# Performance work log

Hardware: AMD Instinct MI355X
Metric: run time of the kernel (lower is better)

The kernel has to match this reference:

```python
import jax, jax.numpy as jnp
import numpy as np

N, E = 100000, 1600000          # nodes, edges
DIN, DH, DOUT = 128, 128, 64    # input_dim, hidden_dim, output_dim


def setup_inputs() -> dict:
    key = jax.random.key(0)
    k0, k1, k2, k3 = jax.random.split(key, 4)
    x = jax.random.normal(k0, (N, DIN), dtype=jnp.float32)
    edge_index = jax.random.randint(k1, (2, E), 0, N)
    # GCNConv params (glorot-ish weights, zero bias)
    W1 = jax.random.normal(k2, (DIN, DH), dtype=jnp.float32) / np.sqrt(DIN).astype(np.float32)
    b1 = jnp.zeros((DH,), jnp.float32)
    W2 = jax.random.normal(k3, (DH, DOUT), dtype=jnp.float32) / np.sqrt(DH).astype(np.float32)
    b2 = jnp.zeros((DOUT,), jnp.float32)
    return {"x": x, "edge_index": edge_index, "W1": W1, "b1": b1, "W2": W2, "b2": b2}


def _gcn_conv(h_in, W, b, src, dst, norm_e, self_norm, n):
    # PyG GCNConv: transform, then normalized sum-aggregation with self-loops.
    h = h_in @ W                                   # [N, dout]
    msg = h[src] * norm_e[:, None]                 # [E, dout] gather + edge scale
    agg = jax.ops.segment_sum(msg, dst, num_segments=n)
    agg = agg + h * self_norm[:, None]             # self-loop contribution (norm = 1/deg)
    return agg + b


def reference(x, edge_index, W1, b1, W2, b2):
    src, dst = edge_index[0], edge_index[1]
    n = x.shape[0]
    # degree including self-loop, computed on dst (PyG convention)
    deg = jax.ops.segment_sum(jnp.ones((src.shape[0],), x.dtype), dst, num_segments=n) + 1.0
    dinv = jax.lax.rsqrt(deg)
    norm_e = dinv[src] * dinv[dst]                 # per-edge D^-1/2 A D^-1/2
    self_norm = dinv * dinv
    h = _gcn_conv(x, W1, b1, src, dst, norm_e, self_norm, n)
    h = jax.nn.relu(h)                             # dropout is identity in eval mode
    out = _gcn_conv(h, W2, b2, src, dst, norm_e, self_norm, n)
    return out
```

## Files before the change

### kernel.cpp

```cpp
#include <hip/hip_runtime.h>

#define NN 100000
#define NE 1600000
#define NBUCK 1563
#define NBH 256
#define CHUNK 6250
#define NSEG 8
#define SEGC (NBH/NSEG)
#define NBXB 12500
#define NBG 1563


typedef short bf16x8 __attribute__((ext_vector_type(8)));
typedef float f32x4  __attribute__((ext_vector_type(4)));
typedef float f32x2  __attribute__((ext_vector_type(2)));

__device__ __forceinline__ float b2f(unsigned short u) {
    return __uint_as_float(((unsigned int)u) << 16);
}
__device__ __forceinline__ unsigned short f2b(float f) {
    unsigned int x = __float_as_uint(f);
    x += 0x7FFFu + ((x >> 16) & 1u);
    return (unsigned short)(x >> 16);
}

__global__ __launch_bounds__(256) void k_pre(const float* __restrict__ x,
                                             unsigned short* __restrict__ xb,
                                             const int* __restrict__ dst,
                                             int* __restrict__ ghist) {
    int b = blockIdx.x;
    if (b < NBXB) {
        int id = b * 256 + threadIdx.x;
        float4 v = ((const float4*)x)[id];
        ushort4 o;
        o.x = f2b(v.x); o.y = f2b(v.y); o.z = f2b(v.z); o.w = f2b(v.w);
        ((ushort4*)xb)[id] = o;
        return;
    }
    __shared__ int h[NBUCK];
    int tid = threadIdx.x;
    int i = b - NBXB;
    for (int k = tid; k < NBUCK; k += 256) h[k] = 0;
    __syncthreads();
    int e0 = i * CHUNK;
    for (int e = e0 + tid; e < e0 + CHUNK; e += 256) {
        unsigned d = (unsigned)dst[e];
        if (d < NN) atomicAdd(&h[d >> 6], 1);
    }
    __syncthreads();
    for (int k = tid; k < NBUCK; k += 256) ghist[i * NBUCK + k] = h[k];
}

__global__ __launch_bounds__(256) void k_scanB(const int* __restrict__ ghist,
                                               int* __restrict__ boffT,
                                               int* __restrict__ tot) {
    __shared__ int part[NSEG][32];
    int kk = threadIdx.x & 31, seg = threadIdx.x >> 5;
    int k = blockIdx.x * 32 + kk;
    bool ok = (k < NBUCK);
    int i0 = seg * SEGC;
    int S = 0;
    if (ok) {
#pragma unroll 8
        for (int i = i0; i < i0 + SEGC; ++i) S += ghist[i * NBUCK + k];
    }
    part[seg][kk] = S;
    __syncthreads();
    int pre = 0;
#pragma unroll
    for (int s2 = 0; s2 < NSEG; ++s2) pre += (s2 < seg) ? part[s2][kk] : 0;
    if (ok) {
        int run = pre;
#pragma unroll 8
        for (int i = i0; i < i0 + SEGC; ++i) {
            int c = ghist[i * NBUCK + k];
            boffT[i * NBUCK + k] = run;
            run += c;
        }
        if (seg == NSEG - 1) tot[k] = run;
    }
}

__global__ __launch_bounds__(256) void k_place(const int* __restrict__ src,
                                               const int* __restrict__ dst,
                                               const int* __restrict__ tot,
                                               const int* __restrict__ boffT,
                                               int* __restrict__ ebuf,
                                               int* __restrict__ bbase_out) {
    __shared__ int cur[NBUCK];
    __shared__ int s[256];
    const int tid = threadIdx.x, bid = blockIdx.x;
    const int i = ((bid & 7) * (NBH / 8)) + (bid >> 3);
    int k0 = tid * 7;
    int v[7]; int S = 0;
#pragma unroll
    for (int q = 0; q < 7; ++q) {
        int k = k0 + q;
        v[q] = (k < NBUCK) ? tot[k] : 0;
        S += v[q];
    }
    s[tid] = S;
    __syncthreads();
    for (int off = 1; off < 256; off <<= 1) {
        int t = (tid >= off) ? s[tid - off] : 0;
        __syncthreads();
        s[tid] += t;
        __syncthreads();
    }
    int run = s[tid] - S;
#pragma unroll
    for (int q = 0; q < 7; ++q) {
        int k = k0 + q;
        if (k < NBUCK) {
            cur[k] = run + boffT[i * NBUCK + k];
            if (bid == 0) bbase_out[k] = run;
            run += v[q];
        }
    }
    __syncthreads();
    int e0 = i * CHUNK;
    for (int e = e0 + tid; e < e0 + CHUNK; e += 256) {
        unsigned d = (unsigned)dst[e];
        if (d >= NN) continue;
        unsigned sv = (unsigned)src[e];
        if (sv >= NN) sv = 0;
        int pos = atomicAdd(&cur[d >> 6], 1);
        ebuf[pos] = (int)(sv | ((d & 63u) << 17));
    }
}

__global__ __launch_bounds__(256) void k_binC(const int* __restrict__ bbase,
                                              const int* __restrict__ tot,
                                              const int* __restrict__ ebuf,
                                              int* __restrict__ row_start,
                                              float* __restrict__ dinv,
                                              int* __restrict__ csr) {
    __shared__ int cnt[64], excl[64], cur[64];
    int b = blockIdx.x, tid = threadIdx.x;
    int n0 = b * 64;
    int base = bbase[b], end = base + tot[b];
    if (tid < 64) cnt[tid] = 0;
    __syncthreads();
    for (int i = base + tid; i < end; i += 256)
        atomicAdd(&cnt[((unsigned)ebuf[i]) >> 17], 1);
    __syncthreads();
    if (tid == 0) {
        int run = 0;
        for (int t = 0; t < 64; ++t) { excl[t] = run; run += cnt[t]; }
    }
    __syncthreads();
    if (tid < 64) {
        int node = n0 + tid;
        if (node < NN) {
            row_start[node] = base + excl[tid];
            dinv[node] = rsqrtf((float)cnt[tid] + 1.0f);
        }
        cur[tid] = base + excl[tid];
    }
    if (b == NBUCK - 1 && tid == 0) row_start[NN] = end;
    __syncthreads();
    for (int i = base + tid; i < end; i += 256) {
        unsigned rec = (unsigned)ebuf[i];
        int pos = atomicAdd(&cur[rec >> 17], 1);
        csr[pos] = (int)(rec & 0x1FFFFu);
    }
}

__global__ __launch_bounds__(256) void k_agg1(const unsigned short* __restrict__ xb,
                                              const float* __restrict__ dinv,
                                              const int* __restrict__ row_start,
                                              const int* __restrict__ csr,
                                              char* __restrict__ P) {
    int node = blockIdx.x * 4 + (threadIdx.x >> 6);
    int lane = threadIdx.x & 63;
    int sub  = lane >> 4;
    int dimb = lane & 15;
    const uint4* X4 = (const uint4*)xb;
    float dv = dinv[node];
    float sn4 = dv * dv * 0.25f;
    uint4 sv = X4[(size_t)node * 16 + dimb];
    f32x2 a0, a1, a2, a3;
    a0.x = __uint_as_float(sv.x << 16) * sn4;  a0.y = __uint_as_float(sv.x & 0xFFFF0000u) * sn4;
    a1.x = __uint_as_float(sv.y << 16) * sn4;  a1.y = __uint_as_float(sv.y & 0xFFFF0000u) * sn4;
    a2.x = __uint_as_float(sv.z << 16) * sn4;  a2.y = __uint_as_float(sv.z & 0xFFFF0000u) * sn4;
    a3.x = __uint_as_float(sv.w << 16) * sn4;  a3.y = __uint_as_float(sv.w & 0xFFFF0000u) * sn4;
    int base = row_start[node], end = row_start[node + 1];
    for (int c0 = base; c0 < end; c0 += 64) {
        int idx = c0 + lane;
        int cl = min(idx, end - 1);
        int s = csr[cl];
        float wv = (idx < end) ? dinv[s] * dv : 0.f;
        int ng = min(64, end - c0);
        for (int g = 0; g * 4 < ng; ++g) {
            int   sq = __shfl(s,  g * 4 + sub);
            float wq = __shfl(wv, g * 4 + sub);
            uint4 v = X4[(size_t)sq * 16 + dimb];
            f32x2 wv2; wv2.x = wq; wv2.y = wq;
            f32x2 xv;
            xv.x = __uint_as_float(v.x << 16); xv.y = __uint_as_float(v.x & 0xFFFF0000u);
            a0 = __builtin_elementwise_fma(xv, wv2, a0);
            xv.x = __uint_as_float(v.y << 16); xv.y = __uint_as_float(v.y & 0xFFFF0000u);
            a1 = __builtin_elementwise_fma(xv, wv2, a1);
            xv.x = __uint_as_float(v.z << 16); xv.y = __uint_as_float(v.z & 0xFFFF0000u);
            a2 = __builtin_elementwise_fma(xv, wv2, a2);
            xv.x = __uint_as_float(v.w << 16); xv.y = __uint_as_float(v.w & 0xFFFF0000u);
            a3 = __builtin_elementwise_fma(xv, wv2, a3);
        }
    }
#pragma unroll
    for (int mgap = 16; mgap < 64; mgap <<= 1) {
        a0.x += __shfl_xor(a0.x, mgap); a0.y += __shfl_xor(a0.y, mgap);
        a1.x += __shfl_xor(a1.x, mgap); a1.y += __shfl_xor(a1.y, mgap);
        a2.x += __shfl_xor(a2.x, mgap); a2.y += __shfl_xor(a2.y, mgap);
        a3.x += __shfl_xor(a3.x, mgap); a3.y += __shfl_xor(a3.y, mgap);
    }
    if (lane < 16) {
        uint4 o;
        o.x = (unsigned)f2b(a0.x) | ((unsigned)f2b(a0.y) << 16);
        o.y = (unsigned)f2b(a1.x) | ((unsigned)f2b(a1.y) << 16);
        o.z = (unsigned)f2b(a2.x) | ((unsigned)f2b(a2.y) << 16);
        o.w = (unsigned)f2b(a3.x) | ((unsigned)f2b(a3.y) << 16);
        ((uint4*)(P + (size_t)node * 256))[lane] = o;
    }
}

__global__ __launch_bounds__(256) void k_gemm12(const float* __restrict__ W1,
                                                const float* __restrict__ b1,
                                                const float* __restrict__ W2,
                                                char* __restrict__ P) {
    __shared__ short Wl1[16384];
    __shared__ short Wl2[8192];
    __shared__ __align__(16) short Cl[4][16][128];
    const int tid = threadIdx.x;
    const int w = tid >> 6, lane = tid & 63;
    const int r0 = blockIdx.x * 64;

    for (int i = tid; i < 16384; i += 256) {
        int j = i & 7, l = (i >> 3) & 63, ks = (i >> 9) & 3, ct = i >> 11;
        int k = ks * 32 + ((l >> 4) << 3) + j;
        int c = ct * 16 + (l & 15);
        Wl1[i] = (short)f2b(W1[k * 128 + c]);
    }
    for (int i = tid; i < 8192; i += 256) {
        int j = i & 7, l = (i >> 3) & 63, ks = (i >> 9) & 3, ct = i >> 11;
        int k = ks * 32 + ((l >> 4) << 3) + j;
        int c = ct * 16 + (l & 15);
        Wl2[i] = (short)f2b(W2[k * 64 + c]);
    }
    __syncthreads();

    const int m = r0 + w * 16 + (lane & 15);
    const int quad = lane >> 4;
    const bool mok = (m < NN);
    bf16x8 a[4];
#pragma unroll
    for (int ks = 0; ks < 4; ++ks) {
        if (mok) a[ks] = *(const bf16x8*)(P + (size_t)m * 256 + (ks * 32 + quad * 8) * 2);
        else     a[ks] = bf16x8{0,0,0,0,0,0,0,0};
    }
#pragma unroll
    for (int ct = 0; ct < 8; ++ct) {
        f32x4 c = {0.f, 0.f, 0.f, 0.f};
#pragma unroll
        for (int ks = 0; ks < 4; ++ks) {
            bf16x8 b = *(const bf16x8*)&Wl1[((ct * 4 + ks) * 64 + lane) * 8];
            c = __builtin_amdgcn_mfma_f32_16x16x32_bf16(a[ks], b, c, 0, 0, 0);
        }
        int col = ct * 16 + (lane & 15);
        float bias = b1[col];
#pragma unroll
        for (int r = 0; r < 4; ++r)
            Cl[w][quad * 4 + r][col] = (short)f2b(fmaxf(c[r] + bias, 0.f));
    }
    __syncthreads();
    bf16x8 a2[4];
#pragma unroll
    for (int ks = 0; ks < 4; ++ks)
        a2[ks] = *(const bf16x8*)&Cl[w][lane & 15][ks * 32 + quad * 8];
    __syncthreads();
    short* Ct = &Cl[0][0][0];
#pragma unroll
    for (int ct = 0; ct < 4; ++ct) {
        f32x4 c = {0.f, 0.f, 0.f, 0.f};
#pragma unroll
        for (int ks = 0; ks < 4; ++ks) {
            bf16x8 b = *(const bf16x8*)&Wl2[((ct * 4 + ks) * 64 + lane) * 8];
            c = __builtin_amdgcn_mfma_f32_16x16x32_bf16(a2[ks], b, c, 0, 0, 0);
        }
        int col = ct * 16 + (lane & 15);
#pragma unroll
        for (int r = 0; r < 4; ++r)
            Ct[(w * 16 + quad * 4 + r) * 64 + col] = (short)f2b(c[r]);
    }
    __syncthreads();
    for (int it = 0; it < 8; ++it) {
        int row = it * 2 + (lane >> 5), u = lane & 31;
        int node = r0 + w * 16 + row;
        if (node < NN)
            *(unsigned int*)(P + (size_t)node * 256 + u * 4) =
                ((const unsigned int*)&Ct[(w * 16 + row) * 64])[u];
    }
}

__global__ __launch_bounds__(256) void k_agg2(const float* __restrict__ dinv,
                                              const int* __restrict__ row_start,
                                              const int* __restrict__ csr,
                                              const char* __restrict__ P,
                                              const float* __restrict__ b2,
                                              float* __restrict__ outp) {
    int node = blockIdx.x * 4 + (threadIdx.x >> 6);
    int lane = threadIdx.x & 63;
    int sub  = lane >> 3;
    int dimb = lane & 7;
    const uint4* P4 = (const uint4*)P;
    float dv = dinv[node];
    float sn8 = dv * dv * 0.125f;
    uint4 sv = P4[(size_t)node * 16 + dimb];
    f32x2 a0, a1, a2, a3;
    a0.x = __uint_as_float(sv.x << 16) * sn8;  a0.y = __uint_as_float(sv.x & 0xFFFF0000u) * sn8;
    a1.x = __uint_as_float(sv.y << 16) * sn8;  a1.y = __uint_as_float(sv.y & 0xFFFF0000u) * sn8;
    a2.x = __uint_as_float(sv.z << 16) * sn8;  a2.y = __uint_as_float(sv.z & 0xFFFF0000u) * sn8;
    a3.x = __uint_as_float(sv.w << 16) * sn8;  a3.y = __uint_as_float(sv.w & 0xFFFF0000u) * sn8;
    int base = row_start[node], end = row_start[node + 1];
    if (end > base) {
        for (int c0 = base; c0 < end; c0 += 64) {
            int idx = c0 + lane;
            int cl = min(idx, end - 1);
            int s = csr[cl];
            float wv = (idx < end) ? dinv[s] * dv : 0.f;
            int ng = min(64, end - c0);
            for (int g = 0; g * 8 < ng; ++g) {
                int   sq = __shfl(s,  g * 8 + sub);
                float wq = __shfl(wv, g * 8 + sub);
                uint4 v = P4[(size_t)sq * 16 + dimb];
                f32x2 wv2; wv2.x = wq; wv2.y = wq;
                f32x2 xv;
                xv.x = __uint_as_float(v.x << 16); xv.y = __uint_as_float(v.x & 0xFFFF0000u);
                a0 = __builtin_elementwise_fma(xv, wv2, a0);
                xv.x = __uint_as_float(v.y << 16); xv.y = __uint_as_float(v.y & 0xFFFF0000u);
                a1 = __builtin_elementwise_fma(xv, wv2, a1);
                xv.x = __uint_as_float(v.z << 16); xv.y = __uint_as_float(v.z & 0xFFFF0000u);
                a2 = __builtin_elementwise_fma(xv, wv2, a2);
                xv.x = __uint_as_float(v.w << 16); xv.y = __uint_as_float(v.w & 0xFFFF0000u);
                a3 = __builtin_elementwise_fma(xv, wv2, a3);
            }
        }
    }
#pragma unroll
    for (int mgap = 8; mgap < 64; mgap <<= 1) {
        a0.x += __shfl_xor(a0.x, mgap); a0.y += __shfl_xor(a0.y, mgap);
        a1.x += __shfl_xor(a1.x, mgap); a1.y += __shfl_xor(a1.y, mgap);
        a2.x += __shfl_xor(a2.x, mgap); a2.y += __shfl_xor(a2.y, mgap);
        a3.x += __shfl_xor(a3.x, mgap); a3.y += __shfl_xor(a3.y, mgap);
    }
    if (lane < 8) {
        float4 ba = ((const float4*)b2)[lane * 2];
        float4 bb = ((const float4*)b2)[lane * 2 + 1];
        float4 o0, o1;
        o0.x = a0.x + ba.x; o0.y = a0.y + ba.y; o0.z = a1.x + ba.z; o0.w = a1.y + ba.w;
        o1.x = a2.x + bb.x; o1.y = a2.y + bb.y; o1.z = a3.x + bb.z; o1.w = a3.y + bb.w;
        ((float4*)outp)[(size_t)node * 16 + lane * 2]     = o0;
        ((float4*)outp)[(size_t)node * 16 + lane * 2 + 1] = o1;
    }
}

extern "C" void kernel_launch(void* const* d_in, const int* in_sizes, int n_in,
                              void* d_out, int out_size, void* d_ws, size_t ws_size,
                              hipStream_t stream) {
    const float* x  = (const float*)d_in[0];
    const int*   ei = (const int*)d_in[1];
    const float* W1 = (const float*)d_in[2];
    const float* b1 = (const float*)d_in[3];
    const float* W2 = (const float*)d_in[4];
    const float* b2 = (const float*)d_in[5];
    float* out = (float*)d_out;
    const int* src = ei;
    const int* dst = ei + NE;

    char* ws = (char*)d_ws;
    unsigned short* xb        = (unsigned short*)(ws + 0);
    char*           P         = ws + 25600000;
    int*            ghist     = (int*)(ws + 25600000);
    int*            boffT     = (int*)(ws + 27200512);
    int*            tot       = (int*)(ws + 28801024);
    int*            bbase     = (int*)(ws + 28807276);
    int*            row_start = (int*)(ws + 51200000);
    float*          dinv      = (float*)(ws + 51600004);
    int*            csr       = (int*)(ws + 52000004);
    int*            ebuf      = (int*)(ws + 58400004);

    k_pre  <<<NBXB + NBH, 256, 0, stream>>>(x, xb, dst, ghist);
    k_scanB<<<(NBUCK + 31) / 32, 256, 0, stream>>>(ghist, boffT, tot);
    k_place<<<NBH, 256, 0, stream>>>(src, dst, tot, boffT, ebuf, bbase);
    k_binC <<<NBUCK, 256, 0, stream>>>(bbase, tot, ebuf, row_start, dinv, csr);

    k_agg1  <<<NN / 4, 256, 0, stream>>>(xb, dinv, row_start, csr, P);
    k_gemm12<<<NBG, 256, 0, stream>>>(W1, b1, W2, P);
    k_agg2  <<<NN / 4, 256, 0, stream>>>(dinv, row_start, csr, P, b2, out);
}
```

Baseline: 311.9 us.

## Make fused GEMM kernel persistent to amortize per-block weight staging

```diff
diff --git a/kernel.cpp b/kernel.cpp
--- a/kernel.cpp
+++ b/kernel.cpp
@@ -9,6 +9,7 @@
 #define SEGC (NBH/NSEG)
 #define NBXB 12500
 #define NBG 1563
+#define NBGG 512
 
 
 typedef short bf16x8 __attribute__((ext_vector_type(8)));
@@ -230,10 +231,10 @@
                                                 char* __restrict__ P) {
     __shared__ short Wl1[16384];
     __shared__ short Wl2[8192];
-    __shared__ __align__(16) short Cl[4][16][128];
+    __shared__ __align__(16) short Cl[4][16][136];
     const int tid = threadIdx.x;
     const int w = tid >> 6, lane = tid & 63;
-    const int r0 = blockIdx.x * 64;
+    const int quad = lane >> 4, l15 = lane & 15;
 
     for (int i = tid; i < 16384; i += 256) {
         int j = i & 7, l = (i >> 3) & 63, ks = (i >> 9) & 3, ct = i >> 11;
@@ -247,58 +248,56 @@
         int c = ct * 16 + (l & 15);
         Wl2[i] = (short)f2b(W2[k * 64 + c]);
     }
-    __syncthreads();
-
-    const int m = r0 + w * 16 + (lane & 15);
-    const int quad = lane >> 4;
-    const bool mok = (m < NN);
-    bf16x8 a[4];
-#pragma unroll
-    for (int ks = 0; ks < 4; ++ks) {
-        if (mok) a[ks] = *(const bf16x8*)(P + (size_t)m * 256 + (ks * 32 + quad * 8) * 2);
-        else     a[ks] = bf16x8{0,0,0,0,0,0,0,0};
-    }
-#pragma unroll
-    for (int ct = 0; ct < 8; ++ct) {
-        f32x4 c = {0.f, 0.f, 0.f, 0.f};
+    float bias1[8];
+#pragma unroll
+    for (int ct = 0; ct < 8; ++ct) bias1[ct] = b1[ct * 16 + l15];
+    __syncthreads();
+
+    for (int t = blockIdx.x; t < NBG; t += NBGG) {
+        const int r0 = t * 64;
+        const int m = r0 + w * 16 + l15;
+        const bool mok = (m < NN);
+        bf16x8 a[4];
 #pragma unroll
         for (int ks = 0; ks < 4; ++ks) {
-            bf16x8 b = *(const bf16x8*)&Wl1[((ct * 4 + ks) * 64 + lane) * 8];
-            c = __builtin_amdgcn_mfma_f32_16x16x32_bf16(a[ks], b, c, 0, 0, 0);
-        }
-        int col = ct * 16 + (lane & 15);
-        float bias = b1[col];
-#pragma unroll
-        for (int r = 0; r < 4; ++r)
-            Cl[w][quad * 4 + r][col] = (short)f2b(fmaxf(c[r] + bias, 0.f));
-    }
-    __syncthreads();
-    bf16x8 a2[4];
-#pragma unroll
-    for (int ks = 0; ks < 4; ++ks)
-        a2[ks] = *(const bf16x8*)&Cl[w][lane & 15][ks * 32 + quad * 8];
-    __syncthreads();
-    short* Ct = &Cl[0][0][0];
-#pragma unroll
-    for (int ct = 0; ct < 4; ++ct) {
-        f32x4 c = {0.f, 0.f, 0.f, 0.f};
-#pragma unroll
-        for (int ks = 0; ks < 4; ++ks) {
-            bf16x8 b = *(const bf16x8*)&Wl2[((ct * 4 + ks) * 64 + lane) * 8];
-            c = __builtin_amdgcn_mfma_f32_16x16x32_bf16(a2[ks], b, c, 0, 0, 0);
-        }
-        int col = ct * 16 + (lane & 15);
-#pragma unroll
-        for (int r = 0; r < 4; ++r)
-            Ct[(w * 16 + quad * 4 + r) * 64 + col] = (short)f2b(c[r]);
-    }
-    __syncthreads();
-    for (int it = 0; it < 8; ++it) {
-        int row = it * 2 + (lane >> 5), u = lane & 31;
-        int node = r0 + w * 16 + row;
-        if (node < NN)
-            *(unsigned int*)(P + (size_t)node * 256 + u * 4) =
-                ((const unsigned int*)&Ct[(w * 16 + row) * 64])[u];
+            if (mok) a[ks] = *(const bf16x8*)(P + (size_t)m * 256 + (ks * 32 + quad * 8) * 2);
+            else     a[ks] = bf16x8{0,0,0,0,0,0,0,0};
+        }
+#pragma unroll
+        for (int ct = 0; ct < 8; ++ct) {
+            f32x4 c = {0.f, 0.f, 0.f, 0.f};
+#pragma unroll
+            for (int ks = 0; ks < 4; ++ks) {
+                bf16x8 b = *(const bf16x8*)&Wl1[((ct * 4 + ks) * 64 + lane) * 8];
+                c = __builtin_amdgcn_mfma_f32_16x16x32_bf16(a[ks], b, c, 0, 0, 0);
+            }
+#pragma unroll
+            for (int r = 0; r < 4; ++r)
+                Cl[w][quad * 4 + r][ct * 16 + l15] =
+                    (short)f2b(fmaxf(c[r] + bias1[ct], 0.f));
+        }
+        __syncthreads();
+        bf16x8 a2[4];
+#pragma unroll
+        for (int ks = 0; ks < 4; ++ks)
+            a2[ks] = *(const bf16x8*)&Cl[w][l15][ks * 32 + quad * 8];
+#pragma unroll
+        for (int ct = 0; ct < 4; ++ct) {
+            f32x4 c = {0.f, 0.f, 0.f, 0.f};
+#pragma unroll
+            for (int ks = 0; ks < 4; ++ks) {
+                bf16x8 b = *(const bf16x8*)&Wl2[((ct * 4 + ks) * 64 + lane) * 8];
+                c = __builtin_amdgcn_mfma_f32_16x16x32_bf16(a2[ks], b, c, 0, 0, 0);
+            }
+#pragma unroll
+            for (int r = 0; r < 4; ++r) {
+                int node = r0 + w * 16 + quad * 4 + r;
+                if (node < NN)
+                    *(unsigned short*)(P + (size_t)node * 256 + (ct * 16 + l15) * 2) =
+                        f2b(c[r]);
+            }
+        }
+        __syncthreads();
     }
 }
 
@@ -395,6 +394,6 @@
     k_binC <<<NBUCK, 256, 0, stream>>>(bbase, tot, ebuf, row_start, dinv, csr);
 
     k_agg1  <<<NN / 4, 256, 0, stream>>>(xb, dinv, row_start, csr, P);
-    k_gemm12<<<NBG, 256, 0, stream>>>(W1, b1, W2, P);
+    k_gemm12<<<NBGG, 256, 0, stream>>>(W1, b1, W2, P);
     k_agg2  <<<NN / 4, 256, 0, stream>>>(dinv, row_start, csr, P, b2, out);
 }
```

After: 293.1 us. -6.0%, faster.
